# Optimization experiments

Measured on AMD Instinct MI355X. Metric: run time of the kernel, lower is better.

## Reference

```python
import jax, jax.numpy as jnp
import numpy as np

N, D, H, E = 50000, 128, 256, 400000


def setup_inputs() -> dict:
    key = jax.random.key(0)
    ks = jax.random.split(key, 10)
    s2d = 1.0 / np.sqrt(2 * D)
    sh = 1.0 / np.sqrt(H)
    return {
        "embeddings": jax.random.normal(ks[0], (N, D), jnp.float32),
        "edge_index": jax.random.randint(ks[1], (2, E), 0, N, jnp.int64),
        # contradiction_detector: Linear(2D,H) -> ReLU -> Linear(H,1) -> Sigmoid
        "Wd1": jax.random.uniform(ks[2], (2 * D, H), jnp.float32, -s2d, s2d),
        "bd1": jax.random.uniform(ks[3], (H,), jnp.float32, -s2d, s2d),
        "Wd2": jax.random.uniform(ks[4], (H, 1), jnp.float32, -sh, sh),
        "bd2": jax.random.uniform(ks[5], (1,), jnp.float32, -sh, sh),
        # resolver: Linear(2D,H) -> ReLU -> Linear(H,D)
        "Wr1": jax.random.uniform(ks[6], (2 * D, H), jnp.float32, -s2d, s2d),
        "br1": jax.random.uniform(ks[7], (H,), jnp.float32, -s2d, s2d),
        "Wr2": jax.random.uniform(ks[8], (H, D), jnp.float32, -sh, sh),
        "br2": jax.random.uniform(ks[9], (D,), jnp.float32, -sh, sh),
    }


def reference(embeddings, edge_index, Wd1, bd1, Wd2, bd2, Wr1, br1, Wr2, br2):
    src, dst = edge_index[0], edge_index[1]
    # gather src/dst features for every edge and concat: (E, 2D)
    pair = jnp.concatenate([embeddings[src], embeddings[dst]], axis=-1)
    # batched detector MLP -> per-edge contradiction score (E,)
    scores = jax.nn.sigmoid(jax.nn.relu(pair @ Wd1 + bd1) @ Wd2 + bd2)[:, 0]
    # batched resolver MLP (depends only on ORIGINAL embeddings): (E, D)
    resolution = jax.nn.relu(pair @ Wr1 + br1) @ Wr2 + br2
    mask = scores > 0.5
    n_edges = src.shape[0]
    n_nodes = embeddings.shape[0]
    # Sequential overwrite semantics: the LAST contradicting edge touching a
    order = jnp.where(mask, jnp.arange(1, n_edges + 1, dtype=jnp.int32), 0)
    last = jnp.zeros((n_nodes,), jnp.int32).at[src].max(order).at[dst].max(order)
    idx = jnp.maximum(last - 1, 0)
    resolved = jnp.where((last > 0)[:, None],
                         (embeddings + resolution[idx]) * 0.5,
                         embeddings)
    return resolved, scores
```

## Files before the change

kernel.cpp:

```cpp
#include <hip/hip_runtime.h>
#include <math.h>

#define NN 50000
#define DD 128
#define K2D 256
#define HH 256
#define EE 400000
#define TE 64
#define RT 32
#define PST 260
#define TAU  0.005f
#define TAU2 5e-5f

typedef __attribute__((ext_vector_type(8))) short bf16x8;
typedef __attribute__((ext_vector_type(4))) float f32x4;
typedef unsigned int uint;
typedef unsigned short ushort;

typedef __attribute__((address_space(3))) void lds_void_t;
typedef __attribute__((address_space(1))) void g1_void_t;

__device__ __forceinline__ ushort f2bf(float x) {
    uint u = __builtin_bit_cast(uint, x);
    u = (u + 0x7FFFu + ((u >> 16) & 1u)) >> 16;
    return (ushort)u;
}

__device__ __forceinline__ int stageOff(int r, int k) {
    return ((r >> 4) * 8 + (k >> 5)) * 512 + ((((k >> 3) & 3) << 4) + (r & 15)) * 8 + (k & 7);
}

__device__ __forceinline__ void swz_unit(const float* __restrict__ W,
                                         ushort* __restrict__ out,
                                         int N, int Kt, int unit, int l)
{
    const int n = unit / Kt, t = unit - n * Kt;
    const int row0 = t * 32 + (l >> 4) * 8;
    const int col = n * 16 + (l & 15);
    ushort tmp[8];
#pragma unroll
    for (int j = 0; j < 8; ++j) tmp[j] = f2bf(W[(row0 + j) * N + col]);
    uint4 p;
    p.x = (uint)tmp[0] | ((uint)tmp[1] << 16);
    p.y = (uint)tmp[2] | ((uint)tmp[3] << 16);
    p.z = (uint)tmp[4] | ((uint)tmp[5] << 16);
    p.w = (uint)tmp[6] | ((uint)tmp[7] << 16);
    *(uint4*)(out + ((size_t)unit * 64 + l) * 8) = p;
}

__global__ __launch_bounds__(256) void prep_kernel(
    const float* __restrict__ emb, ushort* __restrict__ embbf, int doConv,
    const float* __restrict__ Wd1, ushort* __restrict__ wd1s,
    const float* __restrict__ Wr1, ushort* __restrict__ wr1s,
    const float* __restrict__ Wr2, ushort* __restrict__ wr2s)
{
    const int gid = blockIdx.x;
    const int tid = threadIdx.x;
    if (gid < 3125) {
        if (!doConv) return;
        const int i = gid * 256 + tid;
        const float4 a = ((const float4*)emb)[(size_t)i * 2];
        const float4 b = ((const float4*)emb)[(size_t)i * 2 + 1];
        uint4 p;
        p.x = (uint)f2bf(a.x) | ((uint)f2bf(a.y) << 16);
        p.y = (uint)f2bf(a.z) | ((uint)f2bf(a.w) << 16);
        p.z = (uint)f2bf(b.x) | ((uint)f2bf(b.y) << 16);
        p.w = (uint)f2bf(b.z) | ((uint)f2bf(b.w) << 16);
        *(uint4*)(embbf + (size_t)i * 8) = p;
        return;
    }
    const int sub = tid >> 6, l = tid & 63;
    if (gid < 3125 + 32) {
        swz_unit(Wd1, wd1s, HH, 8, (gid - 3125) * 4 + sub, l);
    } else if (gid < 3125 + 64) {
        swz_unit(Wr1, wr1s, HH, 8, (gid - 3125 - 32) * 4 + sub, l);
    } else {
        swz_unit(Wr2, wr2s, DD, 8, (gid - 3125 - 64) * 4 + sub, l);
    }
}

template<int BF>
__global__ __launch_bounds__(256) void det_kernel(
    const float* __restrict__ emb, const ushort* __restrict__ embbf,
    const int* __restrict__ srcIdx, const int* __restrict__ dstIdx,
    const ushort* __restrict__ w1s, const float* __restrict__ b1,
    const float* __restrict__ W2, const float* __restrict__ b2p,
    float* __restrict__ scores,
    int* __restrict__ last,
    int* __restrict__ flagCount, int* __restrict__ flagList, int flagCap)
{
    __shared__ __align__(16) ushort A_lds[TE * K2D];
    __shared__ float zp[256];
    const int tid = threadIdx.x;
    const int e0 = blockIdx.x * TE;
    const int wv = tid >> 6;
    const int lane = tid & 63;

    if (BF) {
        const int r = wv * 16 + (lane & 15);
        const int e = e0 + r;
        const int ns = srcIdx[e], nd = dstIdx[e];
        const int ko = (lane >> 4) * 8;
#pragma unroll
        for (int s = 0; s < 8; ++s) {
            const int node = (s < 4) ? ns : nd;
            const ushort* g = embbf + (size_t)node * DD + (s & 3) * 32 + ko;
            __builtin_amdgcn_global_load_lds((const g1_void_t*)g,
                                             (lds_void_t*)&A_lds[(wv * 8 + s) * 512],
                                             16, 0, 0);
        }
    } else {
        const int r = tid >> 2, q = tid & 3;
        const int e = e0 + r;
        const int node = (q < 2) ? srcIdx[e] : dstIdx[e];
        const float4* s4 = (const float4*)(emb + (size_t)node * DD + (q & 1) * 64);
#pragma unroll
        for (int u = 0; u < 16; ++u) {
            const float4 v = s4[u];
            const int k0 = q * 64 + u * 4;
            uint2 p;
            p.x = (uint)f2bf(v.x) | ((uint)f2bf(v.y) << 16);
            p.y = (uint)f2bf(v.z) | ((uint)f2bf(v.w) << 16);
            *(uint2*)&A_lds[stageOff(r, k0)] = p;
        }
    }
    __syncthreads();

    const int lc = lane & 15, lg = lane >> 4;

    f32x4 acc[4][4] = {};
    const ushort* wbase = w1s + (size_t)(wv * 4) * 8 * 512;

#pragma unroll 2
    for (int t = 0; t < 8; ++t) {
        bf16x8 af[4], bfr[4];
#pragma unroll
        for (int m = 0; m < 4; ++m)
            af[m] = *(const bf16x8*)&A_lds[(m * 8 + t) * 512 + lane * 8];
#pragma unroll
        for (int n = 0; n < 4; ++n)
            bfr[n] = *(const bf16x8*)(wbase + (n * 8 + t) * 512 + lane * 8);
#pragma unroll
        for (int m = 0; m < 4; ++m)
#pragma unroll
            for (int n = 0; n < 4; ++n)
                acc[m][n] = __builtin_amdgcn_mfma_f32_16x16x32_bf16(af[m], bfr[n], acc[m][n], 0, 0, 0);
    }

    float b1v[4], w2v[4];
#pragma unroll
    for (int n = 0; n < 4; ++n) {
        const int col = wv * 64 + n * 16 + lc;
        b1v[n] = b1[col];
        w2v[n] = W2[col];
    }
    float pz[4][4];
#pragma unroll
    for (int m = 0; m < 4; ++m)
#pragma unroll
        for (int r = 0; r < 4; ++r) {
            float s = 0.f;
#pragma unroll
            for (int n = 0; n < 4; ++n)
                s = fmaf(fmaxf(acc[m][n][r] + b1v[n], 0.f), w2v[n], s);
            pz[m][r] = s;
        }
#pragma unroll
    for (int msk = 1; msk <= 8; msk <<= 1)
#pragma unroll
        for (int m = 0; m < 4; ++m)
#pragma unroll
            for (int r = 0; r < 4; ++r)
                pz[m][r] += __shfl_xor(pz[m][r], msk, 64);
    if (lc == 0) {
#pragma unroll
        for (int m = 0; m < 4; ++m)
#pragma unroll
            for (int r = 0; r < 4; ++r)
                zp[wv * 64 + m * 16 + lg * 4 + r] = pz[m][r];
    }
    __syncthreads();

    if (tid < 64) {
        const int e = e0 + tid;
        const float z = zp[tid] + zp[64 + tid] + zp[128 + tid] + zp[192 + tid] + *b2p;
        scores[e] = 1.0f / (1.0f + expf(-z));
        bool deferred = false;
        if (fabsf(z) < TAU) {
            const int slot = atomicAdd(flagCount, 1);
            if (slot < flagCap) { flagList[slot] = e; deferred = true; }
        }
        if (!deferred && z > 0.0f) {
            atomicMax(&last[srcIdx[e]], e + 1);
            atomicMax(&last[dstIdx[e]], e + 1);
        }
    }
}

__global__ __launch_bounds__(256) void refine_kernel(
    const float* __restrict__ emb,
    const int* __restrict__ srcIdx, const int* __restrict__ dstIdx,
    const float* __restrict__ W1, const float* __restrict__ b1,
    const float* __restrict__ W2, const float* __restrict__ b2p,
    int* __restrict__ last,
    const int* __restrict__ flagCount, const int* __restrict__ flagList,
    int flagCap)
{
    __shared__ __align__(16) float P[RT * PST];
    __shared__ int eL[RT];
    __shared__ float zs[RT];
    __shared__ int need64[RT];
    __shared__ double wsumd[4];
    const int tid = threadIdx.x;
    const int cnt = min(*flagCount, flagCap);
    const int nTiles = (cnt + RT - 1) / RT;
    const float b2v = *b2p;

    for (int T = blockIdx.x; T < nTiles; T += gridDim.x) {
        if (tid < RT) {
            const int idx = T * RT + tid;
            eL[tid] = flagList[min(idx, cnt - 1)];
            need64[tid] = 0;
        }
        __syncthreads();
        {
            const int i = tid >> 3, q = tid & 7;
            const int e = eL[i];
            const int node = (q < 4) ? srcIdx[e] : dstIdx[e];
            const float4* s4 = (const float4*)(emb + (size_t)node * DD + (q & 3) * 32);
            float4* d4 = (float4*)(P + i * PST + q * 32);
#pragma unroll
            for (int t = 0; t < 8; ++t) d4[t] = s4[t];
        }
        __syncthreads();

        const int rowg = tid >> 5;
        const int colg = tid & 31;
        const int c0 = colg * 8;

        float acc[4][8];
#pragma unroll
        for (int c = 0; c < 8; ++c) {
            const float bv = b1[c0 + c];
#pragma unroll
            for (int r = 0; r < 4; ++r) acc[r][c] = bv;
        }
        for (int kk = 0; kk < K2D; kk += 4) {
            float af[4][4];
#pragma unroll
            for (int r = 0; r < 4; ++r) {
                const float4 v = *(const float4*)&P[(rowg * 4 + r) * PST + kk];
                af[r][0] = v.x; af[r][1] = v.y; af[r][2] = v.z; af[r][3] = v.w;
            }
#pragma unroll
            for (int dk = 0; dk < 4; ++dk) {
                const float4 w0 = *(const float4*)&W1[(kk + dk) * HH + c0];
                const float4 w1 = *(const float4*)&W1[(kk + dk) * HH + c0 + 4];
#pragma unroll
                for (int r = 0; r < 4; ++r) {
                    const float av = af[r][dk];
                    acc[r][0] = fmaf(av, w0.x, acc[r][0]);
                    acc[r][1] = fmaf(av, w0.y, acc[r][1]);
                    acc[r][2] = fmaf(av, w0.z, acc[r][2]);
                    acc[r][3] = fmaf(av, w0.w, acc[r][3]);
                    acc[r][4] = fmaf(av, w1.x, acc[r][4]);
                    acc[r][5] = fmaf(av, w1.y, acc[r][5]);
                    acc[r][6] = fmaf(av, w1.z, acc[r][6]);
                    acc[r][7] = fmaf(av, w1.w, acc[r][7]);
                }
            }
        }

        float w2[8];
#pragma unroll
        for (int c = 0; c < 8; ++c) w2[c] = W2[c0 + c];
        float pz[4];
#pragma unroll
        for (int r = 0; r < 4; ++r) {
            float s = 0.f;
#pragma unroll
            for (int c = 0; c < 8; ++c) s = fmaf(fmaxf(acc[r][c], 0.f), w2[c], s);
            pz[r] = s;
        }
#pragma unroll
        for (int m = 1; m <= 16; m <<= 1) {
#pragma unroll
            for (int r = 0; r < 4; ++r) pz[r] += __shfl_xor(pz[r], m, 64);
        }
        if (colg == 0) {
#pragma unroll
            for (int r = 0; r < 4; ++r) zs[rowg * 4 + r] = pz[r] + b2v;
        }
        __syncthreads();

        if (tid < RT) {
            const int idx = T * RT + tid;
            if (idx < cnt) {
                const float z = zs[tid];
                if (fabsf(z) < TAU2) {
                    need64[tid] = 1;
                } else if (z > 0.f) {
                    const int e = eL[tid];
                    atomicMax(&last[srcIdx[e]], e + 1);
                    atomicMax(&last[dstIdx[e]], e + 1);
                }
            }
        }
        __syncthreads();

        for (int r = 0; r < RT; ++r) {
            if (!need64[r]) continue;
            const int j = tid;
            double h0 = 0.0, h1 = 0.0;
            for (int k = 0; k < K2D; k += 2) {
                h0 += (double)P[r * PST + k]     * (double)W1[(k)     * HH + j];
                h1 += (double)P[r * PST + k + 1] * (double)W1[(k + 1) * HH + j];
            }
            const double h = (double)b1[j] + h0 + h1;
            double v = (h > 0.0) ? h * (double)W2[j] : 0.0;
#pragma unroll
            for (int m = 1; m <= 32; m <<= 1) v += __shfl_xor(v, m, 64);
            if ((tid & 63) == 0) wsumd[tid >> 6] = v;
            __syncthreads();
            if (tid == 0) {
                const double z = wsumd[0] + wsumd[1] + wsumd[2] + wsumd[3] + (double)b2v;
                if (z > 0.0) {
                    const int e = eL[r];
                    atomicMax(&last[srcIdx[e]], e + 1);
                    atomicMax(&last[dstIdx[e]], e + 1);
                }
            }
            __syncthreads();
        }
        __syncthreads();
    }
}

template<int BF>
__global__ __launch_bounds__(256) void res_kernel(
    const float* __restrict__ emb, const ushort* __restrict__ embbf,
    const int* __restrict__ srcIdx, const int* __restrict__ dstIdx,
    const ushort* __restrict__ w1s, const float* __restrict__ b1,
    const ushort* __restrict__ w2s, const float* __restrict__ b2,
    const int* __restrict__ last,
    float* __restrict__ outRes)
{
    __shared__ __align__(16) ushort A_lds[TE * K2D];
    __shared__ int lastL[TE];
    const int tid = threadIdx.x;
    const int n0 = blockIdx.x * TE;
    const int wv = tid >> 6;
    const int lane = tid & 63;

    if (tid < TE) {
        const int n = n0 + tid;
        lastL[tid] = (n < NN) ? last[n] : 0;
    }
    if (BF) {
        const int r = wv * 16 + (lane & 15);
        const int n = n0 + r;
        int e = 0;
        if (n < NN) { const int lv = last[n]; if (lv > 0) e = lv - 1; }
        const int ns = srcIdx[e], nd = dstIdx[e];
        const int ko = (lane >> 4) * 8;
#pragma unroll
        for (int s = 0; s < 8; ++s) {
            const int node = (s < 4) ? ns : nd;
            const ushort* g = embbf + (size_t)node * DD + (s & 3) * 32 + ko;
            __builtin_amdgcn_global_load_lds((const g1_void_t*)g,
                                             (lds_void_t*)&A_lds[(wv * 8 + s) * 512],
                                             16, 0, 0);
        }
    } else {
        const int r = tid >> 2, q = tid & 3;
        const int n = n0 + r;
        int e = 0;
        if (n < NN) { const int l = last[n]; if (l > 0) e = l - 1; }
        const int node = (q < 2) ? srcIdx[e] : dstIdx[e];
        const float4* s4 = (const float4*)(emb + (size_t)node * DD + (q & 1) * 64);
#pragma unroll
        for (int u = 0; u < 16; ++u) {
            const float4 v = s4[u];
            const int k0 = q * 64 + u * 4;
            uint2 p;
            p.x = (uint)f2bf(v.x) | ((uint)f2bf(v.y) << 16);
            p.y = (uint)f2bf(v.z) | ((uint)f2bf(v.w) << 16);
            *(uint2*)&A_lds[stageOff(r, k0)] = p;
        }
    }
    __syncthreads();

    const int lc = lane & 15, lg = lane >> 4;

    f32x4 acc[4][4] = {};
    {
        const ushort* wbase = w1s + (size_t)(wv * 4) * 8 * 512;
#pragma unroll 2
        for (int t = 0; t < 8; ++t) {
            bf16x8 af[4], bfr[4];
#pragma unroll
            for (int m = 0; m < 4; ++m)
                af[m] = *(const bf16x8*)&A_lds[(m * 8 + t) * 512 + lane * 8];
#pragma unroll
            for (int n = 0; n < 4; ++n)
                bfr[n] = *(const bf16x8*)(wbase + (n * 8 + t) * 512 + lane * 8);
#pragma unroll
            for (int m = 0; m < 4; ++m)
#pragma unroll
                for (int n = 0; n < 4; ++n)
                    acc[m][n] = __builtin_amdgcn_mfma_f32_16x16x32_bf16(af[m], bfr[n], acc[m][n], 0, 0, 0);
        }
    }
    float b1v[4];
#pragma unroll
    for (int n = 0; n < 4; ++n) b1v[n] = b1[wv * 64 + n * 16 + lc];

    __syncthreads();
#pragma unroll
    for (int m = 0; m < 4; ++m)
#pragma unroll
        for (int n = 0; n < 4; ++n) {
            const int hcol = wv * 64 + n * 16 + lc;
#pragma unroll
            for (int r = 0; r < 4; ++r) {
                const int row = m * 16 + lg * 4 + r;
                A_lds[stageOff(row, hcol)] = f2bf(fmaxf(acc[m][n][r] + b1v[n], 0.f));
            }
        }
    __syncthreads();

    f32x4 acc2[4][2] = {};
    {
        const ushort* wbase = w2s + (size_t)(wv * 2) * 8 * 512;
#pragma unroll 2
        for (int t = 0; t < 8; ++t) {
            bf16x8 af[4], bfr[2];
#pragma unroll
            for (int m = 0; m < 4; ++m)
                af[m] = *(const bf16x8*)&A_lds[(m * 8 + t) * 512 + lane * 8];
#pragma unroll
            for (int n = 0; n < 2; ++n)
                bfr[n] = *(const bf16x8*)(wbase + (n * 8 + t) * 512 + lane * 8);
#pragma unroll
            for (int m = 0; m < 4; ++m)
#pragma unroll
                for (int n = 0; n < 2; ++n)
                    acc2[m][n] = __builtin_amdgcn_mfma_f32_16x16x32_bf16(af[m], bfr[n], acc2[m][n], 0, 0, 0);
        }
    }
    float b2v[2];
#pragma unroll
    for (int n = 0; n < 2; ++n) b2v[n] = b2[(wv * 2 + n) * 16 + lc];

#pragma unroll
    for (int m = 0; m < 4; ++m)
#pragma unroll
        for (int r = 0; r < 4; ++r) {
            const int row = m * 16 + lg * 4 + r;
            const int n = n0 + row;
            if (n >= NN) continue;
            const bool hit = lastL[row] > 0;
#pragma unroll
            for (int c = 0; c < 2; ++c) {
                const int col = (wv * 2 + c) * 16 + lc;
                const float ev = emb[(size_t)n * DD + col];
                outRes[(size_t)n * DD + col] =
                    hit ? (ev + acc2[m][c][r] + b2v[c]) * 0.5f : ev;
            }
        }
}

extern "C" void kernel_launch(void* const* d_in, const int* in_sizes, int n_in,
                              void* d_out, int out_size, void* d_ws, size_t ws_size,
                              hipStream_t stream)
{
    const float* emb = (const float*)d_in[0];
    const int*   edge = (const int*)d_in[1];
    const float* Wd1 = (const float*)d_in[2];
    const float* bd1 = (const float*)d_in[3];
    const float* Wd2 = (const float*)d_in[4];
    const float* bd2 = (const float*)d_in[5];
    const float* Wr1 = (const float*)d_in[6];
    const float* br1 = (const float*)d_in[7];
    const float* Wr2 = (const float*)d_in[8];
    const float* br2 = (const float*)d_in[9];

    const int* srcIdx = edge;
    const int* dstIdx = edge + EE;

    float* outRes = (float*)d_out;
    float* scores = outRes + (size_t)NN * DD;

    int* last = (int*)d_ws;
    int* flagCount = last + 50112;
    ushort* wd1s = (ushort*)(last + 50176);
    ushort* wr1s = wd1s + 65536;
    ushort* wr2s = wr1s + 65536;
    int* flagList = (int*)(wr2s + 32768);
    ushort* embbf = (ushort*)(flagList + 65536);

    const size_t base   = 50176u * 4 + (65536u + 65536u + 32768u) * 2 + 65536u * 4;
    const size_t needBF = base + (size_t)NN * DD * 2;
    const int useBF = (ws_size >= needBF) ? 1 : 0;

    int flagCap = 65536;
    if (ws_size < base) {
        long avail = ((long)ws_size - (long)(base - 65536u * 4)) / 4;
        flagCap = avail < 0 ? 0 : (int)avail;
    }

    hipMemsetAsync(d_ws, 0, 50176 * sizeof(int), stream);

    prep_kernel<<<3205, 256, 0, stream>>>(emb, embbf, useBF,
                                          Wd1, wd1s, Wr1, wr1s, Wr2, wr2s);

    if (useBF) {
        det_kernel<1><<<EE / TE, 256, 0, stream>>>(emb, embbf, srcIdx, dstIdx,
                                                   wd1s, bd1, Wd2, bd2,
                                                   scores, last, flagCount, flagList, flagCap);
    } else {
        det_kernel<0><<<EE / TE, 256, 0, stream>>>(emb, embbf, srcIdx, dstIdx,
                                                   wd1s, bd1, Wd2, bd2,
                                                   scores, last, flagCount, flagList, flagCap);
    }
    refine_kernel<<<1024, 256, 0, stream>>>(emb, srcIdx, dstIdx,
                                            Wd1, bd1, Wd2, bd2,
                                            last, flagCount, flagList, flagCap);
    if (useBF) {
        res_kernel<1><<<(NN + TE - 1) / TE, 256, 0, stream>>>(emb, embbf, srcIdx, dstIdx,
                                                              wr1s, br1, wr2s, br2,
                                                              last, outRes);
    } else {
        res_kernel<0><<<(NN + TE - 1) / TE, 256, 0, stream>>>(emb, embbf, srcIdx, dstIdx,
                                                              wr1s, br1, wr2s, br2,
                                                              last, outRes);
    }
}
```

Measured before the change: 199.1 us.

## Make detector kernel persistent with double-buffered async gather into LDS

Replaces the one-tile-per-block detector launch with a persistent grid of 512 blocks that loop over edge tiles. The next tile's bf16 embedding gather is issued into a second LDS buffer with global_load_lds before the current tile's MFMA work, and explicit waitcnt and barriers order the two. Bias and weight vectors are also loaded once per block instead of once per tile. The aim is to hide gather latency behind compute; the cost is double the LDS footprint, which may lower occupancy, and hand-written vmcnt counts that depend on exactly eight outstanding loads.

```diff
diff --git a/kernel.cpp b/kernel.cpp
--- a/kernel.cpp
+++ b/kernel.cpp
@@ -11,6 +11,7 @@
 #define PST 260
 #define TAU  0.005f
 #define TAU2 5e-5f
+#define DGRID 512
 
 typedef __attribute__((ext_vector_type(8))) short bf16x8;
 typedef __attribute__((ext_vector_type(4))) float f32x4;
@@ -79,9 +80,133 @@
     }
 }
 
-template<int BF>
+__global__ __launch_bounds__(256) void det_pipe(
+    const ushort* __restrict__ embbf,
+    const int* __restrict__ srcIdx, const int* __restrict__ dstIdx,
+    const ushort* __restrict__ w1s, const float* __restrict__ b1,
+    const float* __restrict__ W2, const float* __restrict__ b2p,
+    float* __restrict__ scores,
+    int* __restrict__ last,
+    int* __restrict__ flagCount, int* __restrict__ flagList, int flagCap)
+{
+    __shared__ __align__(16) ushort A[2][TE * K2D];
+    __shared__ float zp[2][256];
+    const int tid = threadIdx.x;
+    const int wv = tid >> 6;
+    const int lane = tid & 63;
+    const int lc = lane & 15, lg = lane >> 4;
+    const int nT = EE / TE;
+    const int stride = gridDim.x;
+
+    float b1v[4], w2v[4];
+#pragma unroll
+    for (int n = 0; n < 4; ++n) {
+        const int col = wv * 64 + n * 16 + lc;
+        b1v[n] = b1[col];
+        w2v[n] = W2[col];
+    }
+    const float b2v = *b2p;
+    const ushort* wbase = w1s + (size_t)(wv * 4) * 8 * 512;
+
+    auto STAGE = [&](int T, int bp) {
+        const int e = T * TE + wv * 16 + lc;
+        const int ns = srcIdx[e], nd = dstIdx[e];
+        const int ko = lg * 8;
+#pragma unroll
+        for (int s = 0; s < 8; ++s) {
+            const int node = (s < 4) ? ns : nd;
+            const ushort* g = embbf + (size_t)node * DD + (s & 3) * 32 + ko;
+            __builtin_amdgcn_global_load_lds((const g1_void_t*)g,
+                                             (lds_void_t*)&A[bp][(wv * 8 + s) * 512],
+                                             16, 0, 0);
+        }
+    };
+
+    int T = blockIdx.x;
+    int cur = 0;
+    STAGE(T, 0);
+
+    for (; T < nT; T += stride) {
+        const int Tn = T + stride;
+        if (Tn < nT) {
+            STAGE(Tn, cur ^ 1);
+            asm volatile("s_waitcnt vmcnt(8)" ::: "memory");
+        } else {
+            asm volatile("s_waitcnt vmcnt(0)" ::: "memory");
+        }
+        __builtin_amdgcn_sched_barrier(0);
+        __builtin_amdgcn_s_barrier();
+        __builtin_amdgcn_sched_barrier(0);
+
+        f32x4 acc[4][4] = {};
+#pragma unroll 2
+        for (int t = 0; t < 8; ++t) {
+            bf16x8 af[4], bfr[4];
+#pragma unroll
+            for (int m = 0; m < 4; ++m)
+                af[m] = *(const bf16x8*)&A[cur][(m * 8 + t) * 512 + lane * 8];
+#pragma unroll
+            for (int n = 0; n < 4; ++n)
+                bfr[n] = *(const bf16x8*)(wbase + (n * 8 + t) * 512 + lane * 8);
+#pragma unroll
+            for (int m = 0; m < 4; ++m)
+#pragma unroll
+                for (int n = 0; n < 4; ++n)
+                    acc[m][n] = __builtin_amdgcn_mfma_f32_16x16x32_bf16(af[m], bfr[n], acc[m][n], 0, 0, 0);
+        }
+
+        float pz[4][4];
+#pragma unroll
+        for (int m = 0; m < 4; ++m)
+#pragma unroll
+            for (int r = 0; r < 4; ++r) {
+                float s = 0.f;
+#pragma unroll
+                for (int n = 0; n < 4; ++n)
+                    s = fmaf(fmaxf(acc[m][n][r] + b1v[n], 0.f), w2v[n], s);
+                pz[m][r] = s;
+            }
+#pragma unroll
+        for (int msk = 1; msk <= 8; msk <<= 1)
+#pragma unroll
+            for (int m = 0; m < 4; ++m)
+#pragma unroll
+                for (int r = 0; r < 4; ++r)
+                    pz[m][r] += __shfl_xor(pz[m][r], msk, 64);
+        if (lc == 0) {
+#pragma unroll
+            for (int m = 0; m < 4; ++m)
+#pragma unroll
+                for (int r = 0; r < 4; ++r)
+                    zp[cur][wv * 64 + m * 16 + lg * 4 + r] = pz[m][r];
+        }
+
+        asm volatile("s_waitcnt lgkmcnt(0)" ::: "memory");
+        __builtin_amdgcn_sched_barrier(0);
+        __builtin_amdgcn_s_barrier();
+        __builtin_amdgcn_sched_barrier(0);
+
+        if (tid < 64) {
+            const int e = T * TE + tid;
+            const float z = zp[cur][tid] + zp[cur][64 + tid] +
+                            zp[cur][128 + tid] + zp[cur][192 + tid] + b2v;
+            scores[e] = 1.0f / (1.0f + expf(-z));
+            bool deferred = false;
+            if (fabsf(z) < TAU) {
+                const int slot = atomicAdd(flagCount, 1);
+                if (slot < flagCap) { flagList[slot] = e; deferred = true; }
+            }
+            if (!deferred && z > 0.0f) {
+                atomicMax(&last[srcIdx[e]], e + 1);
+                atomicMax(&last[dstIdx[e]], e + 1);
+            }
+        }
+        cur ^= 1;
+    }
+}
+
 __global__ __launch_bounds__(256) void det_kernel(
-    const float* __restrict__ emb, const ushort* __restrict__ embbf,
+    const float* __restrict__ emb,
     const int* __restrict__ srcIdx, const int* __restrict__ dstIdx,
     const ushort* __restrict__ w1s, const float* __restrict__ b1,
     const float* __restrict__ W2, const float* __restrict__ b2p,
@@ -93,23 +218,7 @@
     __shared__ float zp[256];
     const int tid = threadIdx.x;
     const int e0 = blockIdx.x * TE;
-    const int wv = tid >> 6;
-    const int lane = tid & 63;
-
-    if (BF) {
-        const int r = wv * 16 + (lane & 15);
-        const int e = e0 + r;
-        const int ns = srcIdx[e], nd = dstIdx[e];
-        const int ko = (lane >> 4) * 8;
-#pragma unroll
-        for (int s = 0; s < 8; ++s) {
-            const int node = (s < 4) ? ns : nd;
-            const ushort* g = embbf + (size_t)node * DD + (s & 3) * 32 + ko;
-            __builtin_amdgcn_global_load_lds((const g1_void_t*)g,
-                                             (lds_void_t*)&A_lds[(wv * 8 + s) * 512],
-                                             16, 0, 0);
-        }
-    } else {
+    {
         const int r = tid >> 2, q = tid & 3;
         const int e = e0 + r;
         const int node = (q < 2) ? srcIdx[e] : dstIdx[e];
@@ -126,11 +235,12 @@
     }
     __syncthreads();
 
+    const int wv = tid >> 6;
+    const int lane = tid & 63;
     const int lc = lane & 15, lg = lane >> 4;
 
     f32x4 acc[4][4] = {};
     const ushort* wbase = w1s + (size_t)(wv * 4) * 8 * 512;
-
 #pragma unroll 2
     for (int t = 0; t < 8; ++t) {
         bf16x8 af[4], bfr[4];
@@ -146,7 +256,6 @@
             for (int n = 0; n < 4; ++n)
                 acc[m][n] = __builtin_amdgcn_mfma_f32_16x16x32_bf16(af[m], bfr[n], acc[m][n], 0, 0, 0);
     }
-
     float b1v[4], w2v[4];
 #pragma unroll
     for (int n = 0; n < 4; ++n) {
@@ -180,7 +289,6 @@
                 zp[wv * 64 + m * 16 + lg * 4 + r] = pz[m][r];
     }
     __syncthreads();
-
     if (tid < 64) {
         const int e = e0 + tid;
         const float z = zp[tid] + zp[64 + tid] + zp[128 + tid] + zp[192 + tid] + *b2p;
@@ -515,13 +623,13 @@
                                           Wd1, wd1s, Wr1, wr1s, Wr2, wr2s);
 
     if (useBF) {
-        det_kernel<1><<<EE / TE, 256, 0, stream>>>(emb, embbf, srcIdx, dstIdx,
-                                                   wd1s, bd1, Wd2, bd2,
-                                                   scores, last, flagCount, flagList, flagCap);
+        det_pipe<<<DGRID, 256, 0, stream>>>(embbf, srcIdx, dstIdx,
+                                            wd1s, bd1, Wd2, bd2,
+                                            scores, last, flagCount, flagList, flagCap);
     } else {
-        det_kernel<0><<<EE / TE, 256, 0, stream>>>(emb, embbf, srcIdx, dstIdx,
-                                                   wd1s, bd1, Wd2, bd2,
-                                                   scores, last, flagCount, flagList, flagCap);
+        det_kernel<<<EE / TE, 256, 0, stream>>>(emb, srcIdx, dstIdx,
+                                                wd1s, bd1, Wd2, bd2,
+                                                scores, last, flagCount, flagList, flagCap);
     }
     refine_kernel<<<1024, 256, 0, stream>>>(emb, srcIdx, dstIdx,
                                             Wd1, bd1, Wd2, bd2,
```

Measured after the change: 194.0 us (median of 2 runs). -2.5%, faster.
